# Kernel tuning notes

Hardware: AMD Instinct MI355X
Metric: run time of the kernel (lower is better)

The kernel has to match this reference:

```python
import jax, jax.numpy as jnp
import numpy as np

N_USERS, N_ITEMS, D, F = 100000, 50000, 64, 768
N_NODES = N_USERS + N_ITEMS
N_EDGES = 4800000
BATCH = 4096
LN_EPS = 1e-5
CONTENT_LOSS_W = 0.1


def _layernorm(x):
    # default nn.LayerNorm: weight=1, bias=0
    m = jnp.mean(x, axis=-1, keepdims=True)
    v = jnp.mean(jnp.square(x - m), axis=-1, keepdims=True)
    return (x - m) * jax.lax.rsqrt(v + LN_EPS)


def setup_inputs() -> dict:
    key = jax.random.key(0)
    ks = jax.random.split(key, 12)
    return {
        "users": jax.random.randint(ks[0], (BATCH,), 0, N_USERS),
        "pos_items": jax.random.randint(ks[1], (BATCH,), 0, N_ITEMS),
        "neg_items": jax.random.randint(ks[2], (BATCH,), 0, N_ITEMS),
        "edge_src": jax.random.randint(ks[3], (N_EDGES,), 0, N_NODES, dtype=jnp.int32),
        "edge_dst": jax.random.randint(ks[4], (N_EDGES,), 0, N_NODES, dtype=jnp.int32),
        # symmetric-normalized adjacency values are ~1/deg
        "edge_weight": jax.random.uniform(ks[5], (N_EDGES,), jnp.float32) / 32.0,
        "user_emb": jax.random.normal(ks[6], (N_USERS, D), jnp.float32) * 0.1,
        "item_emb": jax.random.normal(ks[7], (N_ITEMS, D), jnp.float32) * 0.1,
        "content_features": jax.random.normal(ks[8], (N_ITEMS, F), jnp.float32),
        "W_proj": jax.random.normal(ks[9], (F, D), jnp.float32) * 0.02,
        "b_proj": jnp.zeros((D,), jnp.float32),
        "w_gate": jax.random.normal(ks[10], (F,), jnp.float32) * 0.02,
        "b_gate": jnp.zeros((1,), jnp.float32),
        "n_layers": 3,
    }


def reference(users, pos_items, neg_items, edge_src, edge_dst, edge_weight,
              user_emb, item_emb, content_features, W_proj, b_proj,
              w_gate, b_gate, n_layers):
    # gated fusion of collaborative and content item embeddings
    items_content = content_features @ W_proj + b_proj           # [I, D]
    gate = jax.nn.sigmoid(content_features @ w_gate + b_gate)    # [I]
    gate = gate[:, None]
    items = (1.0 - gate) * item_emb + gate * items_content       # [I, D]

    all_emb = jnp.concatenate([user_emb, items], axis=0)          # [N, D]
    acc = all_emb
    emb = all_emb
    for _ in range(n_layers):
        # SpMM: out[dst] += w * emb[src]
        agg = jax.ops.segment_sum(edge_weight[:, None] * emb[edge_src],
                                  edge_dst, num_segments=N_NODES)
        emb = _layernorm(agg) + emb   # LayerNorm + residual
        acc = acc + emb
    light_out = acc / (n_layers + 1)                              # mean over layers

    final_users, final_items = light_out[:N_USERS], light_out[N_USERS:]
    users_out = final_users[users]
    pos_out = final_items[pos_items]
    neg_out = final_items[neg_items]
    content_loss = jnp.mean(jnp.square(final_items - items_content)) * CONTENT_LOSS_W
    return users_out, pos_out, neg_out, content_loss
```

## Files before the change

kernel.cpp:

```cpp
#include <hip/hip_runtime.h>
#include <hip/hip_bf16.h>

#define N_USERS 100000
#define N_ITEMS 50000
#define N_NODES 150000
#define DD 64
#define FF 768
#define N_EDGES_C 4800000
#define BATCH 4096
#define LN_EPS 1e-5f
#define CONTENT_LOSS_W 0.1f

#define NBUCK 147
#define BIN_TILE 4096
#define HIST_BLKS 1200

#define KWIN 24

typedef __attribute__((ext_vector_type(8))) short short8;
typedef __attribute__((ext_vector_type(4))) float f32x4;

__device__ inline float b2f(unsigned short v) {
    union { unsigned int i; float f; } u;
    u.i = ((unsigned int)v) << 16;
    return u.f;
}
__device__ inline unsigned short f2b(float f) {
    union { float f; unsigned int i; } u; u.f = f;
    unsigned int r = u.i + 0x7fff + ((u.i >> 16) & 1);
    return (unsigned short)(r >> 16);
}
__device__ inline short bfc(float f) {
    __hip_bfloat16 h = __float2bfloat16(f);
    return *reinterpret_cast<short*>(&h);
}

__device__ inline uint2 ntld_u2(const uint2* p) {
    unsigned long long v = __builtin_nontemporal_load(
        reinterpret_cast<const unsigned long long*>(p));
    uint2 r; r.x = (unsigned)v; r.y = (unsigned)(v >> 32);
    return r;
}

__global__ __launch_bounds__(256) void init_users_k(
    const float* __restrict__ ue, unsigned short* __restrict__ emb)
{
    int gid = blockIdx.x * 256 + threadIdx.x;
    size_t base = (size_t)gid * 4;
    float4 v = *reinterpret_cast<const float4*>(ue + base);
    ushort4 o;
    o.x = f2b(v.x); o.y = f2b(v.y); o.z = f2b(v.z); o.w = f2b(v.w);
    *reinterpret_cast<ushort4*>(emb + base) = o;
}

__global__ __launch_bounds__(256) void wp_stage_k(
    const float* __restrict__ Wp, unsigned short* __restrict__ bstg)
{
    int tid = blockIdx.x * 256 + threadIdx.x;
    int e    = tid & 7;
    int lane = (tid >> 3) & 63;
    int nt   = (tid >> 9) & 3;
    int kw   = tid >> 11;
    int k = kw * 32 + ((lane >> 4) << 3) + e;
    int n = nt * 16 + (lane & 15);
    bstg[tid] = (unsigned short)bfc(Wp[k * DD + n]);
}

__global__ __launch_bounds__(256) void content_mfma_k(
    const float* __restrict__ cf, const unsigned short* __restrict__ bstg,
    const float* __restrict__ bp, const float* __restrict__ wg,
    const float* __restrict__ bg, const float* __restrict__ item_emb,
    float* __restrict__ items_content,
    unsigned short* __restrict__ emb, float* __restrict__ acc_items)
{
    const int wt = blockIdx.x * 4 + (threadIdx.x >> 6);
    if (wt >= N_ITEMS / 16) return;
    const int lane = threadIdx.x & 63;
    const int row0 = wt * 16;

    const int lrow = lane & 15;
    const int kgrp = lane >> 4;

    const float* aptr = cf + (size_t)(row0 + lrow) * FF + (kgrp << 3);
    const float* wptr = wg + (kgrp << 3);
    const short8* bptr = reinterpret_cast<const short8*>(bstg) + lane;

    f32x4 acc0 = {0.f, 0.f, 0.f, 0.f};
    f32x4 acc1 = {0.f, 0.f, 0.f, 0.f};
    f32x4 acc2 = {0.f, 0.f, 0.f, 0.f};
    f32x4 acc3 = {0.f, 0.f, 0.f, 0.f};
    float gp = 0.f;

    #pragma unroll 4
    for (int kw = 0; kw < KWIN; ++kw) {
        f32x4 a0 = __builtin_nontemporal_load(
            reinterpret_cast<const f32x4*>(aptr + kw * 32));
        f32x4 a1 = __builtin_nontemporal_load(
            reinterpret_cast<const f32x4*>(aptr + kw * 32 + 4));
        float4 w0 = *reinterpret_cast<const float4*>(wptr + kw * 32);
        float4 w1 = *reinterpret_cast<const float4*>(wptr + kw * 32 + 4);

        gp += a0[0] * w0.x + a0[1] * w0.y + a0[2] * w0.z + a0[3] * w0.w;
        gp += a1[0] * w1.x + a1[1] * w1.y + a1[2] * w1.z + a1[3] * w1.w;

        short8 af;
        af[0] = bfc(a0[0]); af[1] = bfc(a0[1]); af[2] = bfc(a0[2]); af[3] = bfc(a0[3]);
        af[4] = bfc(a1[0]); af[5] = bfc(a1[1]); af[6] = bfc(a1[2]); af[7] = bfc(a1[3]);

        const short8* bb = bptr + (size_t)kw * 256;
        short8 b0 = bb[0];
        short8 b1 = bb[64];
        short8 b2 = bb[128];
        short8 b3 = bb[192];

        acc0 = __builtin_amdgcn_mfma_f32_16x16x32_bf16(af, b0, acc0, 0, 0, 0);
        acc1 = __builtin_amdgcn_mfma_f32_16x16x32_bf16(af, b1, acc1, 0, 0, 0);
        acc2 = __builtin_amdgcn_mfma_f32_16x16x32_bf16(af, b2, acc2, 0, 0, 0);
        acc3 = __builtin_amdgcn_mfma_f32_16x16x32_bf16(af, b3, acc3, 0, 0, 0);
    }

    gp += __shfl_xor(gp, 16);
    gp += __shfl_xor(gp, 32);
    const float g = 1.f / (1.f + __expf(-(gp + bg[0])));

    const int rbase = kgrp << 2;
    f32x4 accs[4] = {acc0, acc1, acc2, acc3};
    #pragma unroll
    for (int nt = 0; nt < 4; ++nt) {
        const int col = nt * 16 + lrow;
        const float bpv = bp[col];
        #pragma unroll
        for (int r = 0; r < 4; ++r) {
            const int rit = rbase + r;
            const int row = row0 + rit;
            const float icv = accs[nt][r] + bpv;
            const float gr = __shfl(g, rit);
            const size_t o = (size_t)row * DD + col;
            const float ie = __builtin_nontemporal_load(item_emb + o);
            const float it = (1.f - gr) * ie + gr * icv;
            items_content[o] = icv;
            emb[(size_t)(N_USERS + row) * DD + col] = f2b(it);
            acc_items[o] = it;
        }
    }
}

__global__ __launch_bounds__(256) void bucket_hist_k(
    const int* __restrict__ ed, int* __restrict__ bucket_cnt)
{
    __shared__ int lh[NBUCK];
    for (int i = threadIdx.x; i < NBUCK; i += 256) lh[i] = 0;
    __syncthreads();
    const int stride = HIST_BLKS * 256;
    for (int t = blockIdx.x * 256 + threadIdx.x; t < N_EDGES_C / 4; t += stride) {
        int4 d = reinterpret_cast<const int4*>(ed)[t];
        atomicAdd(&lh[d.x >> 10], 1);
        atomicAdd(&lh[d.y >> 10], 1);
        atomicAdd(&lh[d.z >> 10], 1);
        atomicAdd(&lh[d.w >> 10], 1);
    }
    __syncthreads();
    for (int i = threadIdx.x; i < NBUCK; i += 256) {
        int c = lh[i];
        if (c) atomicAdd(&bucket_cnt[i], c);
    }
}

__global__ __launch_bounds__(256) void bucket_scan_k(
    const int* __restrict__ bucket_cnt, int* __restrict__ bucket_base,
    int* __restrict__ bucket_cursor)
{
    __shared__ int sdata[256];
    int t = threadIdx.x;
    int v = (t < NBUCK) ? bucket_cnt[t] : 0;
    sdata[t] = v;
    __syncthreads();
    for (int off = 1; off < 256; off <<= 1) {
        int x = (t >= off) ? sdata[t - off] : 0;
        __syncthreads();
        sdata[t] += x;
        __syncthreads();
    }
    if (t < NBUCK) {
        int b = sdata[t] - v;
        bucket_base[t] = b;
        bucket_cursor[t] = b;
    }
    if (t == NBUCK - 1) bucket_base[NBUCK] = sdata[t];
}

__global__ __launch_bounds__(256) void bin_k(
    const int* __restrict__ ed, const int* __restrict__ es,
    const float* __restrict__ ew, int* __restrict__ bucket_cursor,
    uint2* __restrict__ binned)
{
    __shared__ uint2 stage[BIN_TILE];
    __shared__ unsigned char bktb[BIN_TILE];
    __shared__ int h[NBUCK];
    __shared__ int o[NBUCK];
    __shared__ int gbase[NBUCK];
    __shared__ int scanbuf[256];

    const int t = threadIdx.x;
    const int base = blockIdx.x * BIN_TILE;
    const int cnt = min(BIN_TILE, N_EDGES_C - base);

    for (int i = t; i < NBUCK; i += 256) h[i] = 0;
    __syncthreads();

    int ld[16]; int ls[16]; float lw[16]; int lb[16];
    #pragma unroll
    for (int k = 0; k < 16; ++k) {
        int i = t + k * 256;
        if (i < cnt) {
            int d = __builtin_nontemporal_load(ed + base + i);
            ld[k] = d;
            ls[k] = __builtin_nontemporal_load(es + base + i);
            lw[k] = __builtin_nontemporal_load(ew + base + i);
            int b = d >> 10;
            lb[k] = b;
            atomicAdd(&h[b], 1);
        } else lb[k] = -1;
    }
    __syncthreads();

    {
        int v = (t < NBUCK) ? h[t] : 0;
        scanbuf[t] = v;
        __syncthreads();
        for (int off = 1; off < 256; off <<= 1) {
            int x = (t >= off) ? scanbuf[t - off] : 0;
            __syncthreads();
            scanbuf[t] += x;
            __syncthreads();
        }
        if (t < NBUCK) o[t] = scanbuf[t] - v;
    }
    __syncthreads();

    if (t < NBUCK) h[t] = o[t];
    __syncthreads();

    #pragma unroll
    for (int k = 0; k < 16; ++k) {
        if (lb[k] >= 0) {
            int p = atomicAdd(&h[lb[k]], 1);
            unsigned key = ((unsigned)ls[k] << 10) | (unsigned)(ld[k] & 1023);
            stage[p] = make_uint2(key, __float_as_uint(lw[k]));
            bktb[p] = (unsigned char)lb[k];
        }
    }
    __syncthreads();

    if (t < NBUCK) {
        int c = h[t] - o[t];
        gbase[t] = (c > 0) ? atomicAdd(&bucket_cursor[t], c) : 0;
    }
    __syncthreads();

    for (int i = t; i < cnt; i += 256) {
        int b = bktb[i];
        binned[gbase[b] + (i - o[b])] = stage[i];
    }
}

__global__ __launch_bounds__(1024) void scatter_k(
    const uint2* __restrict__ binned, const int* __restrict__ bucket_base,
    int* __restrict__ cursor, uint2* __restrict__ adj)
{
    __shared__ int lh[1024];
    __shared__ int sdata[1024];
    const int b = blockIdx.x;
    const int t = threadIdx.x;
    const int nb = b << 10;
    const int s0 = bucket_base[b];
    const int s1 = bucket_base[b + 1];

    lh[t] = 0;
    __syncthreads();
    for (int i = s0 + t; i < s1; i += 1024)
        atomicAdd(&lh[binned[i].x & 1023u], 1);
    __syncthreads();

    int v = lh[t];
    sdata[t] = v;
    __syncthreads();
    for (int off = 1; off < 1024; off <<= 1) {
        int x = (t >= off) ? sdata[t - off] : 0;
        __syncthreads();
        sdata[t] += x;
        __syncthreads();
    }
    const int start = s0 + sdata[t] - v;
    if (nb + t < N_NODES) cursor[nb + t] = start;
    lh[t] = start;
    __syncthreads();

    for (int i = s0 + t; i < s1; i += 1024) {
        uint2 e = binned[i];
        int ln = (int)(e.x & 1023u);
        int p = atomicAdd(&lh[ln], 1);
        adj[p] = make_uint2(e.x >> 10, e.y);
    }
}

__global__ __launch_bounds__(256) void agg_ln_k(
    const unsigned short* __restrict__ emb_in,
    unsigned short* __restrict__ emb_out,
    float* __restrict__ acc_items,
    const int* __restrict__ cursor, const uint2* __restrict__ adj)
{
    const int n = blockIdx.x * 4 + (threadIdx.x >> 6);
    const int lane = threadIdx.x & 63;
    const int g = lane >> 4;
    const int q = lane & 15;
    const int qo = q << 2;

    const int beg = cursor[n];
    const int end = (n == N_NODES - 1) ? N_EDGES_C : cursor[n + 1];

    float a0 = 0.f, a1 = 0.f, a2 = 0.f, a3 = 0.f;

    int j = beg;
    for (; j + 31 < end; j += 32) {
        uint2 e0 = ntld_u2(&adj[j      + g]);
        uint2 e1 = ntld_u2(&adj[j +  4 + g]);
        uint2 e2 = ntld_u2(&adj[j +  8 + g]);
        uint2 e3 = ntld_u2(&adj[j + 12 + g]);
        uint2 e4 = ntld_u2(&adj[j + 16 + g]);
        uint2 e5 = ntld_u2(&adj[j + 20 + g]);
        uint2 e6 = ntld_u2(&adj[j + 24 + g]);
        uint2 e7 = ntld_u2(&adj[j + 28 + g]);
        ushort4 r0 = *reinterpret_cast<const ushort4*>(emb_in + (size_t)e0.x * DD + qo);
        ushort4 r1 = *reinterpret_cast<const ushort4*>(emb_in + (size_t)e1.x * DD + qo);
        ushort4 r2 = *reinterpret_cast<const ushort4*>(emb_in + (size_t)e2.x * DD + qo);
        ushort4 r3 = *reinterpret_cast<const ushort4*>(emb_in + (size_t)e3.x * DD + qo);
        ushort4 r4 = *reinterpret_cast<const ushort4*>(emb_in + (size_t)e4.x * DD + qo);
        ushort4 r5 = *reinterpret_cast<const ushort4*>(emb_in + (size_t)e5.x * DD + qo);
        ushort4 r6 = *reinterpret_cast<const ushort4*>(emb_in + (size_t)e6.x * DD + qo);
        ushort4 r7 = *reinterpret_cast<const ushort4*>(emb_in + (size_t)e7.x * DD + qo);
        float w0 = __uint_as_float(e0.y), w1 = __uint_as_float(e1.y);
        float w2 = __uint_as_float(e2.y), w3 = __uint_as_float(e3.y);
        float w4 = __uint_as_float(e4.y), w5 = __uint_as_float(e5.y);
        float w6 = __uint_as_float(e6.y), w7 = __uint_as_float(e7.y);
        a0 += w0 * b2f(r0.x); a1 += w0 * b2f(r0.y); a2 += w0 * b2f(r0.z); a3 += w0 * b2f(r0.w);
        a0 += w1 * b2f(r1.x); a1 += w1 * b2f(r1.y); a2 += w1 * b2f(r1.z); a3 += w1 * b2f(r1.w);
        a0 += w2 * b2f(r2.x); a1 += w2 * b2f(r2.y); a2 += w2 * b2f(r2.z); a3 += w2 * b2f(r2.w);
        a0 += w3 * b2f(r3.x); a1 += w3 * b2f(r3.y); a2 += w3 * b2f(r3.z); a3 += w3 * b2f(r3.w);
        a0 += w4 * b2f(r4.x); a1 += w4 * b2f(r4.y); a2 += w4 * b2f(r4.z); a3 += w4 * b2f(r4.w);
        a0 += w5 * b2f(r5.x); a1 += w5 * b2f(r5.y); a2 += w5 * b2f(r5.z); a3 += w5 * b2f(r5.w);
        a0 += w6 * b2f(r6.x); a1 += w6 * b2f(r6.y); a2 += w6 * b2f(r6.z); a3 += w6 * b2f(r6.w);
        a0 += w7 * b2f(r7.x); a1 += w7 * b2f(r7.y); a2 += w7 * b2f(r7.z); a3 += w7 * b2f(r7.w);
    }
    if (j + 15 < end) {
        uint2 e0 = ntld_u2(&adj[j + g]);
        uint2 e1 = ntld_u2(&adj[j + 4 + g]);
        uint2 e2 = ntld_u2(&adj[j + 8 + g]);
        uint2 e3 = ntld_u2(&adj[j + 12 + g]);
        ushort4 r0 = *reinterpret_cast<const ushort4*>(emb_in + (size_t)e0.x * DD + qo);
        ushort4 r1 = *reinterpret_cast<const ushort4*>(emb_in + (size_t)e1.x * DD + qo);
        ushort4 r2 = *reinterpret_cast<const ushort4*>(emb_in + (size_t)e2.x * DD + qo);
        ushort4 r3 = *reinterpret_cast<const ushort4*>(emb_in + (size_t)e3.x * DD + qo);
        float w0 = __uint_as_float(e0.y), w1 = __uint_as_float(e1.y);
        float w2 = __uint_as_float(e2.y), w3 = __uint_as_float(e3.y);
        a0 += w0 * b2f(r0.x); a1 += w0 * b2f(r0.y); a2 += w0 * b2f(r0.z); a3 += w0 * b2f(r0.w);
        a0 += w1 * b2f(r1.x); a1 += w1 * b2f(r1.y); a2 += w1 * b2f(r1.z); a3 += w1 * b2f(r1.w);
        a0 += w2 * b2f(r2.x); a1 += w2 * b2f(r2.y); a2 += w2 * b2f(r2.z); a3 += w2 * b2f(r2.w);
        a0 += w3 * b2f(r3.x); a1 += w3 * b2f(r3.y); a2 += w3 * b2f(r3.z); a3 += w3 * b2f(r3.w);
        j += 16;
    }
    for (; j + 3 < end; j += 4) {
        uint2 e = ntld_u2(&adj[j + g]);
        ushort4 r = *reinterpret_cast<const ushort4*>(emb_in + (size_t)e.x * DD + qo);
        float w = __uint_as_float(e.y);
        a0 += w * b2f(r.x); a1 += w * b2f(r.y); a2 += w * b2f(r.z); a3 += w * b2f(r.w);
    }
    if (g < end - j) {
        uint2 e = ntld_u2(&adj[j + g]);
        ushort4 r = *reinterpret_cast<const ushort4*>(emb_in + (size_t)e.x * DD + qo);
        float w = __uint_as_float(e.y);
        a0 += w * b2f(r.x); a1 += w * b2f(r.y); a2 += w * b2f(r.z); a3 += w * b2f(r.w);
    }

    a0 += __shfl_xor(a0, 16); a0 += __shfl_xor(a0, 32);
    a1 += __shfl_xor(a1, 16); a1 += __shfl_xor(a1, 32);
    a2 += __shfl_xor(a2, 16); a2 += __shfl_xor(a2, 32);
    a3 += __shfl_xor(a3, 16); a3 += __shfl_xor(a3, 32);

    float s = a0 + a1 + a2 + a3;
    s += __shfl_xor(s, 1); s += __shfl_xor(s, 2);
    s += __shfl_xor(s, 4); s += __shfl_xor(s, 8);
    const float m = s * (1.f / 64.f);
    const float d0 = a0 - m, d1 = a1 - m, d2 = a2 - m, d3 = a3 - m;
    float vv = d0 * d0 + d1 * d1 + d2 * d2 + d3 * d3;
    vv += __shfl_xor(vv, 1); vv += __shfl_xor(vv, 2);
    vv += __shfl_xor(vv, 4); vv += __shfl_xor(vv, 8);
    const float rstd = rsqrtf(vv * (1.f / 64.f) + LN_EPS);

    if (g == 0) {
        const size_t o = (size_t)n * DD + qo;
        ushort4 own = *reinterpret_cast<const ushort4*>(emb_in + o);
        float e0 = d0 * rstd + b2f(own.x);
        float e1 = d1 * rstd + b2f(own.y);
        float e2 = d2 * rstd + b2f(own.z);
        float e3 = d3 * rstd + b2f(own.w);
        ushort4 ob;
        ob.x = f2b(e0); ob.y = f2b(e1); ob.z = f2b(e2); ob.w = f2b(e3);
        *reinterpret_cast<ushort4*>(emb_out + o) = ob;
        if (n >= N_USERS) {
            float4* ap = reinterpret_cast<float4*>(
                acc_items + (size_t)(n - N_USERS) * DD + qo);
            float4 v = *ap;
            v.x += e0; v.y += e1; v.z += e2; v.w += e3;
            *ap = v;
        }
    }
}

__global__ __launch_bounds__(256) void gather_acc_k(
    const int* __restrict__ users, const int* __restrict__ pos,
    const int* __restrict__ neg, const unsigned short* __restrict__ emb_state,
    float* __restrict__ out, int init)
{
    int gid = blockIdx.x * 256 + threadIdx.x;
    int part = gid / (BATCH * DD);
    int r = gid - part * (BATCH * DD);
    int b = r >> 6, c = r & 63;
    int node;
    if (part == 0)      node = users[b];
    else if (part == 1) node = N_USERS + pos[b];
    else                node = N_USERS + neg[b];
    float v = b2f(emb_state[(size_t)node * DD + c]);
    if (init) out[gid] = v;
    else      out[gid] += v;
}

__global__ __launch_bounds__(256) void loss_k(
    const float* __restrict__ acc_items, const float* __restrict__ ic,
    float* __restrict__ loss_slot)
{
    const int total = N_ITEMS * DD;
    int stride = gridDim.x * 256;
    float p = 0.f;
    for (int i = blockIdx.x * 256 + threadIdx.x; i < total; i += stride) {
        float d = __builtin_nontemporal_load(acc_items + i) * 0.25f
                - __builtin_nontemporal_load(ic + i);
        p += d * d;
    }
    #pragma unroll
    for (int off = 32; off; off >>= 1) p += __shfl_xor(p, off);
    __shared__ float red[4];
    if ((threadIdx.x & 63) == 0) red[threadIdx.x >> 6] = p;
    __syncthreads();
    if (threadIdx.x == 0)
        atomicAdd(loss_slot, red[0] + red[1] + red[2] + red[3]);
}

__global__ __launch_bounds__(256) void final_out_k(
    const float* __restrict__ loss_slot, float* __restrict__ out)
{
    int gid = blockIdx.x * 256 + threadIdx.x;
    out[gid] *= 0.25f;
    if (gid == 0)
        out[3 * BATCH * DD] =
            loss_slot[0] * (CONTENT_LOSS_W / (float)(N_ITEMS * DD));
}

extern "C" void kernel_launch(void* const* d_in, const int* in_sizes, int n_in,
                              void* d_out, int out_size, void* d_ws, size_t ws_size,
                              hipStream_t stream)
{
    const int* users = (const int*)d_in[0];
    const int* pos   = (const int*)d_in[1];
    const int* neg   = (const int*)d_in[2];
    const int* es    = (const int*)d_in[3];
    const int* ed    = (const int*)d_in[4];
    const float* ew  = (const float*)d_in[5];
    const float* ue  = (const float*)d_in[6];
    const float* ie  = (const float*)d_in[7];
    const float* cf  = (const float*)d_in[8];
    const float* Wp  = (const float*)d_in[9];
    const float* bp  = (const float*)d_in[10];
    const float* wg  = (const float*)d_in[11];
    const float* bg  = (const float*)d_in[12];
    float* out = (float*)d_out;

    unsigned short* embA = (unsigned short*)d_ws;
    unsigned short* embB = embA + (size_t)N_NODES * DD;
    float* acc_items = (float*)(embB + (size_t)N_NODES * DD);
    float* ic        = acc_items + (size_t)N_ITEMS * DD;
    float* loss_slot = ic + (size_t)N_ITEMS * DD;
    int*   cursor    = (int*)(loss_slot + 16);
    int*   bucket_cnt    = cursor + 150016;
    int*   bucket_base   = bucket_cnt + 256;
    int*   bucket_cursor = bucket_base + 256;
    uint2* adj       = (uint2*)(bucket_cursor + 256);
    uint2* binned    = (uint2*)embB;
    unsigned short* bstg = embA;

    hipMemsetAsync(bucket_cnt, 0, 256 * sizeof(int), stream);
    hipMemsetAsync(loss_slot, 0, sizeof(float), stream);

    bucket_hist_k<<<HIST_BLKS, 256, 0, stream>>>(ed, bucket_cnt);
    bucket_scan_k<<<1, 256, 0, stream>>>(bucket_cnt, bucket_base, bucket_cursor);
    bin_k<<<(N_EDGES_C + BIN_TILE - 1) / BIN_TILE, 256, 0, stream>>>(
        ed, es, ew, bucket_cursor, binned);
    scatter_k<<<NBUCK, 1024, 0, stream>>>(binned, bucket_base, cursor, adj);

    wp_stage_k<<<192, 256, 0, stream>>>(Wp, bstg);
    content_mfma_k<<<(N_ITEMS / 16 + 3) / 4, 256, 0, stream>>>(
        cf, bstg, bp, wg, bg, ie, ic, embA, acc_items);
    init_users_k<<<(N_USERS * DD / 4) / 256, 256, 0, stream>>>(ue, embA);
    gather_acc_k<<<3 * BATCH * DD / 256, 256, 0, stream>>>(users, pos, neg,
                                                           embA, out, 1);

    unsigned short* cur = embA;
    unsigned short* nxt = embB;
    for (int l = 0; l < 3; ++l) {
        agg_ln_k<<<N_NODES / 4, 256, 0, stream>>>(cur, nxt, acc_items,
                                                  cursor, adj);
        gather_acc_k<<<3 * BATCH * DD / 256, 256, 0, stream>>>(users, pos, neg,
                                                               nxt, out, 0);
        unsigned short* t = cur; cur = nxt; nxt = t;
    }

    loss_k<<<2048, 256, 0, stream>>>(acc_items, ic, loss_slot);
    final_out_k<<<3 * BATCH * DD / 256, 256, 0, stream>>>(loss_slot, out);
}
```

Measured before the change: 882.9 us.

## Fuse histogram with user init, use wave-shuffle scan, drop nontemporal adj loads

Merges the edge bucket histogram and the user-embedding bf16 conversion into one launch by splitting blocks between the two tasks. The W_proj staging buffer moves to embB so it no longer overlaps the user rows now written early into embA. The 1024-wide shared-memory Hillis-Steele scan in scatter_k becomes a two-level wavefront shuffle scan with fewer barriers. Adjacency loads in the aggregation kernel switch from nontemporal to normal loads, which changes cache behaviour for the reused CSR.

```diff
diff --git a/kernel.cpp b/kernel.cpp
--- a/kernel.cpp
+++ b/kernel.cpp
@@ -14,6 +14,7 @@
 #define NBUCK 147
 #define BIN_TILE 4096
 #define HIST_BLKS 1200
+#define INIT_BLKS 6250
 
 #define KWIN 24
 
@@ -35,22 +36,36 @@
     return *reinterpret_cast<short*>(&h);
 }
 
-__device__ inline uint2 ntld_u2(const uint2* p) {
-    unsigned long long v = __builtin_nontemporal_load(
-        reinterpret_cast<const unsigned long long*>(p));
-    uint2 r; r.x = (unsigned)v; r.y = (unsigned)(v >> 32);
-    return r;
-}
-
-__global__ __launch_bounds__(256) void init_users_k(
+
+__global__ __launch_bounds__(256) void prep_k(
+    const int* __restrict__ ed, int* __restrict__ bucket_cnt,
     const float* __restrict__ ue, unsigned short* __restrict__ emb)
 {
-    int gid = blockIdx.x * 256 + threadIdx.x;
-    size_t base = (size_t)gid * 4;
-    float4 v = *reinterpret_cast<const float4*>(ue + base);
-    ushort4 o;
-    o.x = f2b(v.x); o.y = f2b(v.y); o.z = f2b(v.z); o.w = f2b(v.w);
-    *reinterpret_cast<ushort4*>(emb + base) = o;
+    __shared__ int lh[NBUCK];
+    if (blockIdx.x < HIST_BLKS) {
+        for (int i = threadIdx.x; i < NBUCK; i += 256) lh[i] = 0;
+        __syncthreads();
+        const int stride = HIST_BLKS * 256;
+        for (int t = blockIdx.x * 256 + threadIdx.x; t < N_EDGES_C / 4; t += stride) {
+            int4 d = reinterpret_cast<const int4*>(ed)[t];
+            atomicAdd(&lh[d.x >> 10], 1);
+            atomicAdd(&lh[d.y >> 10], 1);
+            atomicAdd(&lh[d.z >> 10], 1);
+            atomicAdd(&lh[d.w >> 10], 1);
+        }
+        __syncthreads();
+        for (int i = threadIdx.x; i < NBUCK; i += 256) {
+            int c = lh[i];
+            if (c) atomicAdd(&bucket_cnt[i], c);
+        }
+    } else {
+        int gid = (blockIdx.x - HIST_BLKS) * 256 + threadIdx.x;
+        size_t base = (size_t)gid * 4;
+        float4 v = *reinterpret_cast<const float4*>(ue + base);
+        ushort4 o;
+        o.x = f2b(v.x); o.y = f2b(v.y); o.z = f2b(v.z); o.w = f2b(v.w);
+        *reinterpret_cast<ushort4*>(emb + base) = o;
+    }
 }
 
 __global__ __launch_bounds__(256) void wp_stage_k(
@@ -145,27 +160,6 @@
     }
 }
 
-__global__ __launch_bounds__(256) void bucket_hist_k(
-    const int* __restrict__ ed, int* __restrict__ bucket_cnt)
-{
-    __shared__ int lh[NBUCK];
-    for (int i = threadIdx.x; i < NBUCK; i += 256) lh[i] = 0;
-    __syncthreads();
-    const int stride = HIST_BLKS * 256;
-    for (int t = blockIdx.x * 256 + threadIdx.x; t < N_EDGES_C / 4; t += stride) {
-        int4 d = reinterpret_cast<const int4*>(ed)[t];
-        atomicAdd(&lh[d.x >> 10], 1);
-        atomicAdd(&lh[d.y >> 10], 1);
-        atomicAdd(&lh[d.z >> 10], 1);
-        atomicAdd(&lh[d.w >> 10], 1);
-    }
-    __syncthreads();
-    for (int i = threadIdx.x; i < NBUCK; i += 256) {
-        int c = lh[i];
-        if (c) atomicAdd(&bucket_cnt[i], c);
-    }
-}
-
 __global__ __launch_bounds__(256) void bucket_scan_k(
     const int* __restrict__ bucket_cnt, int* __restrict__ bucket_base,
     int* __restrict__ bucket_cursor)
@@ -269,9 +263,11 @@
     int* __restrict__ cursor, uint2* __restrict__ adj)
 {
     __shared__ int lh[1024];
-    __shared__ int sdata[1024];
+    __shared__ int wsum[16];
     const int b = blockIdx.x;
     const int t = threadIdx.x;
+    const int lane = t & 63;
+    const int wid = t >> 6;
     const int nb = b << 10;
     const int s0 = bucket_base[b];
     const int s1 = bucket_base[b + 1];
@@ -282,16 +278,27 @@
         atomicAdd(&lh[binned[i].x & 1023u], 1);
     __syncthreads();
 
-    int v = lh[t];
-    sdata[t] = v;
-    __syncthreads();
-    for (int off = 1; off < 1024; off <<= 1) {
-        int x = (t >= off) ? sdata[t - off] : 0;
-        __syncthreads();
-        sdata[t] += x;
-        __syncthreads();
-    }
-    const int start = s0 + sdata[t] - v;
+    const int v = lh[t];
+    int x = v;
+    #pragma unroll
+    for (int off = 1; off < 64; off <<= 1) {
+        int y = __shfl_up(x, off);
+        if (lane >= off) x += y;
+    }
+    if (lane == 63) wsum[wid] = x;
+    __syncthreads();
+    if (wid == 0 && lane < 16) {
+        int w = wsum[lane];
+        #pragma unroll
+        for (int off = 1; off < 16; off <<= 1) {
+            int y = __shfl_up(w, off);
+            if (lane >= off) w += y;
+        }
+        wsum[lane] = w;
+    }
+    __syncthreads();
+    const int wbase = (wid > 0) ? wsum[wid - 1] : 0;
+    const int start = s0 + wbase + (x - v);
     if (nb + t < N_NODES) cursor[nb + t] = start;
     lh[t] = start;
     __syncthreads();
@@ -323,14 +330,14 @@
 
     int j = beg;
     for (; j + 31 < end; j += 32) {
-        uint2 e0 = ntld_u2(&adj[j      + g]);
-        uint2 e1 = ntld_u2(&adj[j +  4 + g]);
-        uint2 e2 = ntld_u2(&adj[j +  8 + g]);
-        uint2 e3 = ntld_u2(&adj[j + 12 + g]);
-        uint2 e4 = ntld_u2(&adj[j + 16 + g]);
-        uint2 e5 = ntld_u2(&adj[j + 20 + g]);
-        uint2 e6 = ntld_u2(&adj[j + 24 + g]);
-        uint2 e7 = ntld_u2(&adj[j + 28 + g]);
+        uint2 e0 = adj[j      + g];
+        uint2 e1 = adj[j +  4 + g];
+        uint2 e2 = adj[j +  8 + g];
+        uint2 e3 = adj[j + 12 + g];
+        uint2 e4 = adj[j + 16 + g];
+        uint2 e5 = adj[j + 20 + g];
+        uint2 e6 = adj[j + 24 + g];
+        uint2 e7 = adj[j + 28 + g];
         ushort4 r0 = *reinterpret_cast<const ushort4*>(emb_in + (size_t)e0.x * DD + qo);
         ushort4 r1 = *reinterpret_cast<const ushort4*>(emb_in + (size_t)e1.x * DD + qo);
         ushort4 r2 = *reinterpret_cast<const ushort4*>(emb_in + (size_t)e2.x * DD + qo);
@@ -353,10 +360,10 @@
         a0 += w7 * b2f(r7.x); a1 += w7 * b2f(r7.y); a2 += w7 * b2f(r7.z); a3 += w7 * b2f(r7.w);
     }
     if (j + 15 < end) {
-        uint2 e0 = ntld_u2(&adj[j + g]);
-        uint2 e1 = ntld_u2(&adj[j + 4 + g]);
-        uint2 e2 = ntld_u2(&adj[j + 8 + g]);
-        uint2 e3 = ntld_u2(&adj[j + 12 + g]);
+        uint2 e0 = adj[j + g];
+        uint2 e1 = adj[j + 4 + g];
+        uint2 e2 = adj[j + 8 + g];
+        uint2 e3 = adj[j + 12 + g];
         ushort4 r0 = *reinterpret_cast<const ushort4*>(emb_in + (size_t)e0.x * DD + qo);
         ushort4 r1 = *reinterpret_cast<const ushort4*>(emb_in + (size_t)e1.x * DD + qo);
         ushort4 r2 = *reinterpret_cast<const ushort4*>(emb_in + (size_t)e2.x * DD + qo);
@@ -370,13 +377,13 @@
         j += 16;
     }
     for (; j + 3 < end; j += 4) {
-        uint2 e = ntld_u2(&adj[j + g]);
+        uint2 e = adj[j + g];
         ushort4 r = *reinterpret_cast<const ushort4*>(emb_in + (size_t)e.x * DD + qo);
         float w = __uint_as_float(e.y);
         a0 += w * b2f(r.x); a1 += w * b2f(r.y); a2 += w * b2f(r.z); a3 += w * b2f(r.w);
     }
     if (g < end - j) {
-        uint2 e = ntld_u2(&adj[j + g]);
+        uint2 e = adj[j + g];
         ushort4 r = *reinterpret_cast<const ushort4*>(emb_in + (size_t)e.x * DD + qo);
         float w = __uint_as_float(e.y);
         a0 += w * b2f(r.x); a1 += w * b2f(r.y); a2 += w * b2f(r.z); a3 += w * b2f(r.w);
@@ -496,12 +503,13 @@
     int*   bucket_cursor = bucket_base + 256;
     uint2* adj       = (uint2*)(bucket_cursor + 256);
     uint2* binned    = (uint2*)embB;
-    unsigned short* bstg = embA;
+    unsigned short* bstg = embB;
 
     hipMemsetAsync(bucket_cnt, 0, 256 * sizeof(int), stream);
     hipMemsetAsync(loss_slot, 0, sizeof(float), stream);
 
-    bucket_hist_k<<<HIST_BLKS, 256, 0, stream>>>(ed, bucket_cnt);
+    prep_k<<<HIST_BLKS + INIT_BLKS, 256, 0, stream>>>(ed, bucket_cnt, ue, embA);
+
     bucket_scan_k<<<1, 256, 0, stream>>>(bucket_cnt, bucket_base, bucket_cursor);
     bin_k<<<(N_EDGES_C + BIN_TILE - 1) / BIN_TILE, 256, 0, stream>>>(
         ed, es, ew, bucket_cursor, binned);
@@ -510,7 +518,6 @@
     wp_stage_k<<<192, 256, 0, stream>>>(Wp, bstg);
     content_mfma_k<<<(N_ITEMS / 16 + 3) / 4, 256, 0, stream>>>(
         cf, bstg, bp, wg, bg, ie, ic, embA, acc_items);
-    init_users_k<<<(N_USERS * DD / 4) / 256, 256, 0, stream>>>(ue, embA);
     gather_acc_k<<<3 * BATCH * DD / 256, 256, 0, stream>>>(users, pos, neg,
                                                            embA, out, 1);
 
```

Result: faster. 808.2 us (-8.5%).
